# Performance work log

Hardware: AMD Instinct MI355X
Metric: run time of the kernel (lower is better)

Reference implementation:

```python
import jax, jax.numpy as jnp
import numpy as np

HEAD_NUMS = 8
LN_EPS = 1e-5


def _layernorm(x, g, b):
    m = jnp.mean(x, axis=-1, keepdims=True)
    v = jnp.var(x, axis=-1, keepdims=True)
    return (x - m) * jax.lax.rsqrt(v + LN_EPS) * g + b


def setup_inputs() -> dict:
    key = jax.random.key(0)
    ks = jax.random.split(key, 6)
    B, S, D = 4, 2048, 512
    x = jax.random.normal(ks[0], (B, S, D), dtype=jnp.float32)
    W1 = jax.random.normal(ks[1], (4 * D, D), dtype=jnp.float32) * 0.02
    b1 = jnp.zeros((4 * D,), dtype=jnp.float32)
    ln_g = jnp.ones((D,), dtype=jnp.float32)
    ln_b = jnp.zeros((D,), dtype=jnp.float32)
    W2 = jax.random.normal(ks[2], (D, D), dtype=jnp.float32) * 0.02
    b2 = jnp.zeros((D,), dtype=jnp.float32)
    return {"x": x, "W1": W1, "b1": b1, "ln_g": ln_g, "ln_b": ln_b, "W2": W2, "b2": b2}


def reference(x, W1, b1, ln_g, ln_b, W2, b2):
    B, S, D = x.shape
    H = HEAD_NUMS
    hd = D // H
    # fused qkv+gate projection with SiLU (HSTU style)
    h = jax.nn.silu(x @ W1.T + b1)                   # [B,S,4D]
    h = h.reshape(B, S, 4, H, hd)                    # split into gate,q,k,v
    gate = jnp.transpose(h[:, :, 0], (0, 2, 1, 3))   # [B,H,S,hd]
    q = jnp.transpose(h[:, :, 1], (0, 2, 1, 3))
    k = jnp.transpose(h[:, :, 2], (0, 2, 1, 3))
    v = jnp.transpose(h[:, :, 3], (0, 2, 1, 3))
    scale = 1.0 / np.sqrt(hd).astype(np.float32)
    scores = jnp.einsum('bhsd,bhtd->bhst', q, k) * scale   # [B,H,S,S]
    causal = jnp.tril(jnp.ones((S, S), dtype=bool))        # allowed: t <= s
    # silu replaces softmax; masked (future) positions contribute 0
    # (mathematical limit of silu(-inf) is 0)
    a = jnp.where(causal, jax.nn.silu(scores), 0.0)
    o = jnp.einsum('bhst,bhtd->bhsd', a, v)                # [B,H,S,hd]
    o = jnp.transpose(o, (0, 2, 1, 3)).reshape(B, S, D)
    normed = _layernorm(o, ln_g, ln_b)
    gate_f = jnp.transpose(gate, (0, 2, 1, 3)).reshape(B, S, D)
    return (normed * gate_f) @ W2.T + b2
```

## Files before the change

kernel.cpp:

```cpp
#include <hip/hip_runtime.h>
#include <hip/hip_bf16.h>
#include <cstdint>


typedef __attribute__((ext_vector_type(8))) short short8;
typedef __attribute__((ext_vector_type(4))) float f32x4;

__device__ __forceinline__ unsigned short f2bf(float f) {
  union { float f; unsigned u; } v; v.f = f;
  unsigned r = v.u + 0x7FFFu + ((v.u >> 16) & 1u);
  return (unsigned short)(r >> 16);
}
__device__ __forceinline__ float bf2f(unsigned short h) {
  union { unsigned u; float f; } v; v.u = ((unsigned)h) << 16; return v.f;
}
__device__ __forceinline__ float fast_rcp(float x) {
#if __has_builtin(__builtin_amdgcn_rcpf)
  return __builtin_amdgcn_rcpf(x);
#else
  return 1.0f / x;
#endif
}
__device__ __forceinline__ float fast_exp2(float x) {
#if __has_builtin(__builtin_amdgcn_exp2f)
  return __builtin_amdgcn_exp2f(x);
#else
  return exp2f(x);
#endif
}
__device__ __forceinline__ float silu_f(float x) {
  return x * fast_rcp(1.0f + fast_exp2(-1.442695041f * x));
}
__device__ __forceinline__ unsigned pk2(float lo, float hi) {
  union { __hip_bfloat162 b; unsigned u; } cv;
  cv.b = __float22bfloat162_rn(make_float2(lo, hi));
  return cv.u;
}
__device__ __forceinline__ void gl_lds16(const void* g, void* l) {
  __builtin_amdgcn_global_load_lds(
      (const __attribute__((address_space(1))) void*)g,
      (__attribute__((address_space(3))) void*)l, 16, 0, 0);
}

__global__ void convert_kernel(const float* __restrict__ x, const float* __restrict__ w1,
                               const float* __restrict__ w2,
                               unsigned short* __restrict__ xb, unsigned short* __restrict__ w1b,
                               unsigned short* __restrict__ w2b) {
  int i = blockIdx.x * 256 + threadIdx.x;
  const float* s; unsigned short* d;
  if (i < 1048576) { s = x; d = xb; }
  else if (i < 1048576 + 262144) { i -= 1048576; s = w1; d = w1b; }
  else { i -= (1048576 + 262144); if (i >= 65536) return; s = w2; d = w2b; }
  float4 f = ((const float4*)s)[i];
  uint2 o; o.x = pk2(f.x, f.y); o.y = pk2(f.z, f.w);
  ((uint2*)d)[i] = o;
}

__global__ __launch_bounds__(256, 2) void gemm1_kernel(
    const unsigned short* __restrict__ xb,
    const unsigned short* __restrict__ w1b,
    const float* __restrict__ b1,
    unsigned short* __restrict__ h,
    unsigned short* __restrict__ vt)
{
  __shared__ __align__(16) unsigned short smem[16896];
  unsigned short* As = smem;
  unsigned short* Bs = smem + 8192;
  const int tid = threadIdx.x;
  const int w = tid >> 6, l = tid & 63;
  const int bm = blockIdx.x & 63, bn = blockIdx.x >> 6;
  const int wm = w & 1, wn = w >> 1;
  const int quad = l >> 4, lc = l & 15, lc7 = lc & 7;
  const int r8 = l >> 3, c8 = (l & 7) ^ r8;

  f32x4 acc[4][4] = {};
  const unsigned short* ga = xb + (size_t)(bm * 128 + w * 32 + r8) * 512 + c8 * 8;
  const unsigned short* gb = w1b + (size_t)(bn * 128 + w * 32 + r8) * 512 + c8 * 8;

  for (int kt = 0; kt < 512; kt += 64) {
#pragma unroll
    for (int i = 0; i < 4; ++i) {
      gl_lds16(ga + i * 8 * 512 + kt, As + (w * 4 + i) * 512);
      gl_lds16(gb + i * 8 * 512 + kt, Bs + (w * 4 + i) * 512);
    }
    __syncthreads();
#pragma unroll
    for (int kk = 0; kk < 2; ++kk) {
      short8 af[4], bf[4];
#pragma unroll
      for (int mt = 0; mt < 4; ++mt)
        af[mt] = *(const short8*)(As + (wm * 64 + mt * 16 + lc) * 64 +
                                  (((kk * 4 + quad) ^ lc7) * 8));
#pragma unroll
      for (int nt = 0; nt < 4; ++nt)
        bf[nt] = *(const short8*)(Bs + (wn * 64 + nt * 16 + lc) * 64 +
                                  (((kk * 4 + quad) ^ lc7) * 8));
#pragma unroll
      for (int mt = 0; mt < 4; ++mt)
#pragma unroll
        for (int nt = 0; nt < 4; ++nt)
          acc[mt][nt] = __builtin_amdgcn_mfma_f32_16x16x32_bf16(af[mt], bf[nt], acc[mt][nt], 0, 0, 0);
    }
    __syncthreads();
  }

  unsigned short* T = smem;
  const int sec = bn >> 2;
  if (sec == 3) {
#pragma unroll
    for (int nt = 0; nt < 4; ++nt) {
      const int nl = wn * 64 + nt * 16 + lc;
      const float bias = b1[bn * 128 + nl];
#pragma unroll
      for (int mt = 0; mt < 4; ++mt) {
        const int sl = wm * 64 + mt * 16 + quad * 4;
        uint2 pk;
        pk.x = pk2(silu_f(acc[mt][nt][0] + bias), silu_f(acc[mt][nt][1] + bias));
        pk.y = pk2(silu_f(acc[mt][nt][2] + bias), silu_f(acc[mt][nt][3] + bias));
        *(uint2*)(T + nl * 132 + sl) = pk;
      }
    }
  } else {
    const float osc = (sec == 1) ? 0.125f : 1.0f;
#pragma unroll
    for (int nt = 0; nt < 4; ++nt) {
      const int nl = wn * 64 + nt * 16 + lc;
      const float bias = b1[bn * 128 + nl];
#pragma unroll
      for (int mt = 0; mt < 4; ++mt) {
        const int sl = wm * 64 + mt * 16 + quad * 4;
#pragma unroll
        for (int r = 0; r < 4; ++r)
          T[(sl + r) * 132 + nl] = f2bf(silu_f(acc[mt][nt][r] + bias) * osc);
      }
    }
  }
  __syncthreads();
  const int rrow = tid >> 4, rcol = (tid & 15) * 8;
  if (sec == 3) {
    const int bq = bm >> 4, sbase = (bm & 15) * 128;
#pragma unroll
    for (int p = 0; p < 8; ++p) {
      const int row = p * 16 + rrow;
      const int n = bn * 128 + row, hh = (n >> 6) & 7, d = n & 63;
      *(short8*)(vt + (size_t)((bq * 8 + hh) * 64 + d) * 2048 + sbase + rcol) =
          *(const short8*)(T + row * 132 + rcol);
    }
  } else {
#pragma unroll
    for (int p = 0; p < 8; ++p) {
      const int row = p * 16 + rrow;
      *(short8*)(h + (size_t)(bm * 128 + row) * 2048 + bn * 128 + rcol) =
          *(const short8*)(T + row * 132 + rcol);
    }
  }
}

__global__ __launch_bounds__(256, 3) void attn_kernel(
    const unsigned short* __restrict__ h,
    const unsigned short* __restrict__ vt,
    float* __restrict__ o)
{
  __shared__ __align__(16) unsigned short Ks[128 * 64];
  __shared__ __align__(16) unsigned short Vs[64 * 128];
  __shared__ __align__(16) unsigned short Ps[64 * 136];
  const int tid = threadIdx.x;
  const int w = tid >> 6, l = tid & 63;
  const int bh = blockIdx.x & 31;
  const int qi = 31 - (blockIdx.x >> 5);
  const int b = bh >> 3, hh = bh & 7;
  const int quad = l >> 4, lc = l & 15, lc7 = lc & 7;
  const int r8 = l >> 3, c8 = (l & 7) ^ r8;
  const int wm = w & 1, wn = w >> 1;
  const int q0 = qi * 64;
  const int nk = (qi >> 1) + 1;

  {
    const unsigned short* qg =
        h + (size_t)(b * 2048 + q0 + w * 16 + r8) * 2048 + 512 + hh * 64 + c8 * 8;
#pragma unroll
    for (int i = 0; i < 2; ++i)
      gl_lds16(qg + (size_t)i * 8 * 2048, Ks + (w * 2 + i) * 512);
  }
  __syncthreads();
  short8 qf[2][2];
#pragma unroll
  for (int nt = 0; nt < 2; ++nt)
#pragma unroll
    for (int kk = 0; kk < 2; ++kk)
      qf[nt][kk] = *(const short8*)(Ks + (wn * 32 + nt * 16 + lc) * 64 +
                                    (((kk * 4 + quad) ^ lc7) * 8));

  f32x4 oacc[4] = {};

  const unsigned short* kg =
      h + (size_t)(b * 2048 + w * 32 + r8) * 2048 + 1024 + hh * 64 + c8 * 8;
  const int vrow = l >> 4, vcol = l & 15;
  const unsigned short* vgE =
      vt + (size_t)(bh * 64 + w * 16 + vrow) * 2048 + ((vcol ^ vrow) * 8);
  const unsigned short* vgO =
      vt + (size_t)(bh * 64 + w * 16 + vrow) * 2048 + ((vcol ^ vrow ^ 4) * 8);

  for (int ti = 0; ti < nk; ++ti) {
    __syncthreads();
    const int toff = ti * 128;
#pragma unroll
    for (int i = 0; i < 4; ++i) {
      gl_lds16(kg + (size_t)(toff + i * 8) * 2048, Ks + (w * 4 + i) * 512);
      const unsigned short* vsrc = ((i & 1) ? vgO : vgE) + (size_t)(i * 4) * 2048 + toff;
      gl_lds16(vsrc, Vs + (w * 4 + i) * 512);
    }
    __syncthreads();

    f32x4 sc[4][2] = {};
#pragma unroll
    for (int kk = 0; kk < 2; ++kk) {
      short8 kf[4];
#pragma unroll
      for (int mt = 0; mt < 4; ++mt)
        kf[mt] = *(const short8*)(Ks + (wm * 64 + mt * 16 + lc) * 64 +
                                  (((kk * 4 + quad) ^ lc7) * 8));
#pragma unroll
      for (int mt = 0; mt < 4; ++mt)
#pragma unroll
        for (int nt = 0; nt < 2; ++nt)
          sc[mt][nt] = __builtin_amdgcn_mfma_f32_16x16x32_bf16(kf[mt], qf[nt][kk], sc[mt][nt], 0, 0, 0);
    }

    if (ti < nk - 1) {
#pragma unroll
      for (int mt = 0; mt < 4; ++mt) {
        const int tloc = wm * 64 + mt * 16 + quad * 4;
#pragma unroll
        for (int nt = 0; nt < 2; ++nt) {
          const int qloc = wn * 32 + nt * 16 + lc;
          uint2 pk;
          pk.x = pk2(silu_f(sc[mt][nt][0]), silu_f(sc[mt][nt][1]));
          pk.y = pk2(silu_f(sc[mt][nt][2]), silu_f(sc[mt][nt][3]));
          *(uint2*)(Ps + qloc * 136 + tloc) = pk;
        }
      }
    } else {
#pragma unroll
      for (int mt = 0; mt < 4; ++mt) {
        const int tloc = wm * 64 + mt * 16 + quad * 4;
        const int tg = toff + tloc;
#pragma unroll
        for (int nt = 0; nt < 2; ++nt) {
          const int qloc = wn * 32 + nt * 16 + lc;
          const int qg = q0 + qloc;
          float v0 = (tg + 0 <= qg) ? silu_f(sc[mt][nt][0]) : 0.0f;
          float v1 = (tg + 1 <= qg) ? silu_f(sc[mt][nt][1]) : 0.0f;
          float v2 = (tg + 2 <= qg) ? silu_f(sc[mt][nt][2]) : 0.0f;
          float v3 = (tg + 3 <= qg) ? silu_f(sc[mt][nt][3]) : 0.0f;
          uint2 pk; pk.x = pk2(v0, v1); pk.y = pk2(v2, v3);
          *(uint2*)(Ps + qloc * 136 + tloc) = pk;
        }
      }
    }
    __syncthreads();

#pragma unroll
    for (int ks = 0; ks < 4; ++ks) {
      short8 pf = *(const short8*)(Ps + (w * 16 + lc) * 136 + ks * 32 + quad * 8);
#pragma unroll
      for (int nt = 0; nt < 4; ++nt) {
        short8 vf = *(const short8*)(Vs + (nt * 16 + lc) * 128 +
                                     (((ks * 4 + quad) ^ lc7) * 8));
        oacc[nt] = __builtin_amdgcn_mfma_f32_16x16x32_bf16(pf, vf, oacc[nt], 0, 0, 0);
      }
    }
  }

  float* og = o + (size_t)(b * 2048 + q0 + w * 16) * 512 + hh * 64;
#pragma unroll
  for (int nt = 0; nt < 4; ++nt)
#pragma unroll
    for (int r = 0; r < 4; ++r)
      og[(quad * 4 + r) * 512 + nt * 16 + lc] = oacc[nt][r];
}

__global__ __launch_bounds__(256) void ln_gate_kernel(
    const float* __restrict__ o, const unsigned short* __restrict__ h,
    const float* __restrict__ lng, const float* __restrict__ lnb,
    unsigned short* __restrict__ y) {
  const int row = blockIdx.x * 4 + (threadIdx.x >> 6);
  const int l = threadIdx.x & 63;
  const float4* orow = (const float4*)(o + (size_t)row * 512);
  float4 a = orow[l * 2], c = orow[l * 2 + 1];
  float s0 = a.x + a.y + a.z + a.w + c.x + c.y + c.z + c.w;
#pragma unroll
  for (int off = 32; off > 0; off >>= 1) s0 += __shfl_xor(s0, off);
  const float mean = s0 * (1.0f / 512.0f);
  float dx[8] = {a.x - mean, a.y - mean, a.z - mean, a.w - mean,
                 c.x - mean, c.y - mean, c.z - mean, c.w - mean};
  float sq = 0.f;
#pragma unroll
  for (int j = 0; j < 8; ++j) sq += dx[j] * dx[j];
#pragma unroll
  for (int off = 32; off > 0; off >>= 1) sq += __shfl_xor(sq, off);
  const float inv = rsqrtf(sq * (1.0f / 512.0f) + 1e-5f);
  const float4* g4 = (const float4*)lng;
  const float4* b4 = (const float4*)lnb;
  float4 g0 = g4[l * 2], g1 = g4[l * 2 + 1], bb0 = b4[l * 2], bb1 = b4[l * 2 + 1];
  const unsigned short* grow = h + (size_t)row * 2048;
  ushort4 gr0 = *(const ushort4*)(grow + l * 8);
  ushort4 gr1 = *(const ushort4*)(grow + l * 8 + 4);
  float gg[8] = {g0.x, g0.y, g0.z, g0.w, g1.x, g1.y, g1.z, g1.w};
  float bbv[8] = {bb0.x, bb0.y, bb0.z, bb0.w, bb1.x, bb1.y, bb1.z, bb1.w};
  float gv[8] = {bf2f(gr0.x), bf2f(gr0.y), bf2f(gr0.z), bf2f(gr0.w),
                 bf2f(gr1.x), bf2f(gr1.y), bf2f(gr1.z), bf2f(gr1.w)};
  float r[8];
#pragma unroll
  for (int j = 0; j < 8; ++j) r[j] = (dx[j] * inv * gg[j] + bbv[j]) * gv[j];
  uint2 p0, p1;
  p0.x = pk2(r[0], r[1]); p0.y = pk2(r[2], r[3]);
  p1.x = pk2(r[4], r[5]); p1.y = pk2(r[6], r[7]);
  uint2* yrow = (uint2*)(y + (size_t)row * 512);
  yrow[l * 2] = p0;
  yrow[l * 2 + 1] = p1;
}

__global__ __launch_bounds__(256, 2) void gemm2_kernel(
    const unsigned short* __restrict__ yb,
    const unsigned short* __restrict__ w2b,
    const float* __restrict__ b2, float* __restrict__ out) {
  __shared__ __align__(16) unsigned short As[128 * 64];
  __shared__ __align__(16) unsigned short Bs[128 * 64];
  const int tid = threadIdx.x;
  const int w = tid >> 6, l = tid & 63;
  const int bm = blockIdx.x & 63, bn = blockIdx.x >> 6;
  const int wm = w & 1, wn = w >> 1;
  const int quad = l >> 4, lc = l & 15, lc7 = lc & 7;
  const int r8 = l >> 3, c8 = (l & 7) ^ r8;

  f32x4 acc[4][4] = {};
  const unsigned short* ga = yb + (size_t)(bm * 128 + w * 32 + r8) * 512 + c8 * 8;
  const unsigned short* gb = w2b + (size_t)(bn * 128 + w * 32 + r8) * 512 + c8 * 8;

  for (int kt = 0; kt < 512; kt += 64) {
#pragma unroll
    for (int i = 0; i < 4; ++i) {
      gl_lds16(ga + i * 8 * 512 + kt, As + (w * 4 + i) * 512);
      gl_lds16(gb + i * 8 * 512 + kt, Bs + (w * 4 + i) * 512);
    }
    __syncthreads();
#pragma unroll
    for (int kk = 0; kk < 2; ++kk) {
      short8 af[4], bf[4];
#pragma unroll
      for (int mt = 0; mt < 4; ++mt)
        af[mt] = *(const short8*)(As + (wm * 64 + mt * 16 + lc) * 64 +
                                  (((kk * 4 + quad) ^ lc7) * 8));
#pragma unroll
      for (int nt = 0; nt < 4; ++nt)
        bf[nt] = *(const short8*)(Bs + (wn * 64 + nt * 16 + lc) * 64 +
                                  (((kk * 4 + quad) ^ lc7) * 8));
#pragma unroll
      for (int mt = 0; mt < 4; ++mt)
#pragma unroll
        for (int nt = 0; nt < 4; ++nt)
          acc[mt][nt] = __builtin_amdgcn_mfma_f32_16x16x32_bf16(af[mt], bf[nt], acc[mt][nt], 0, 0, 0);
    }
    __syncthreads();
  }

#pragma unroll
  for (int nt = 0; nt < 4; ++nt) {
    const int n = bn * 128 + wn * 64 + nt * 16 + lc;
    const float bias = b2[n];
#pragma unroll
    for (int mt = 0; mt < 4; ++mt) {
      const int m0 = bm * 128 + wm * 64 + mt * 16 + quad * 4;
#pragma unroll
      for (int r = 0; r < 4; ++r)
        out[(size_t)(m0 + r) * 512 + n] = acc[mt][nt][r] + bias;
    }
  }
}

extern "C" void kernel_launch(void* const* d_in, const int* in_sizes, int n_in,
                              void* d_out, int out_size, void* d_ws, size_t ws_size,
                              hipStream_t stream) {
  const float* x = (const float*)d_in[0];
  const float* W1 = (const float*)d_in[1];
  const float* b1 = (const float*)d_in[2];
  const float* lng = (const float*)d_in[3];
  const float* lnb = (const float*)d_in[4];
  const float* W2 = (const float*)d_in[5];
  const float* b2 = (const float*)d_in[6];
  float* out = (float*)d_out;
  char* ws = (char*)d_ws;

  unsigned short* xb  = (unsigned short*)(ws);
  unsigned short* w1b = (unsigned short*)(ws + 8388608);
  unsigned short* w2b = (unsigned short*)(ws + 10485760);
  unsigned short* h   = (unsigned short*)(ws + 11010048);
  unsigned short* vt  = (unsigned short*)(ws + 44564480);
  float* o            = (float*)(ws + 52953088);
  unsigned short* yb  = (unsigned short*)(ws + 69730304);

  convert_kernel<<<5376, 256, 0, stream>>>(x, W1, W2, xb, w1b, w2b);
  gemm1_kernel<<<1024, 256, 0, stream>>>(xb, w1b, b1, h, vt);
  attn_kernel<<<1024, 256, 0, stream>>>(h, vt, o);
  ln_gate_kernel<<<2048, 256, 0, stream>>>(o, h, lng, lnb, yb);
  gemm2_kernel<<<256, 256, 0, stream>>>(yb, w2b, b2, out);
}
```

Measured before the change: 158.9 us.

## Register-prefetch next K/V tile in attention; shrink gemm2 tiles for more blocks

In the attention kernel, the direct global-to-LDS loads of K and V are replaced by a register prefetch. The next tile's K and V are loaded into registers while the current tile is computed, then written to LDS at the start of the next iteration. This is meant to hide global load latency behind the MFMA and SiLU work, at the cost of extra VGPRs and an extra register-to-LDS store. Separately, gemm2 uses 64x128 tiles with 512 blocks instead of 128x128 with 256, to better fill the CUs for this small GEMM at the cost of less reuse per block.

```diff
diff --git a/kernel.cpp b/kernel.cpp
--- a/kernel.cpp
+++ b/kernel.cpp
@@ -193,24 +193,39 @@
 
   f32x4 oacc[4] = {};
 
-  const unsigned short* kg =
+  const unsigned short* kgl =
       h + (size_t)(b * 2048 + w * 32 + r8) * 2048 + 1024 + hh * 64 + c8 * 8;
   const int vrow = l >> 4, vcol = l & 15;
-  const unsigned short* vgE =
-      vt + (size_t)(bh * 64 + w * 16 + vrow) * 2048 + ((vcol ^ vrow) * 8);
-  const unsigned short* vgO =
-      vt + (size_t)(bh * 64 + w * 16 + vrow) * 2048 + ((vcol ^ vrow ^ 4) * 8);
+  const unsigned short* vgl[4];
+#pragma unroll
+  for (int i = 0; i < 4; ++i) {
+    const int d = w * 16 + i * 4 + vrow;
+    vgl[i] = vt + (size_t)(bh * 64 + d) * 2048 + ((vcol ^ (d & 7)) * 8);
+  }
+
+  short8 kreg[4], vreg[4];
+#pragma unroll
+  for (int i = 0; i < 4; ++i) {
+    kreg[i] = *(const short8*)(kgl + (size_t)(i * 8) * 2048);
+    vreg[i] = *(const short8*)(vgl[i]);
+  }
 
   for (int ti = 0; ti < nk; ++ti) {
     __syncthreads();
-    const int toff = ti * 128;
 #pragma unroll
     for (int i = 0; i < 4; ++i) {
-      gl_lds16(kg + (size_t)(toff + i * 8) * 2048, Ks + (w * 4 + i) * 512);
-      const unsigned short* vsrc = ((i & 1) ? vgO : vgE) + (size_t)(i * 4) * 2048 + toff;
-      gl_lds16(vsrc, Vs + (w * 4 + i) * 512);
-    }
-    __syncthreads();
+      *(short8*)(Ks + (w * 4 + i) * 512 + l * 8) = kreg[i];
+      *(short8*)(Vs + (w * 4 + i) * 512 + l * 8) = vreg[i];
+    }
+    __syncthreads();
+    if (ti + 1 < nk) {
+      const int toff = (ti + 1) * 128;
+#pragma unroll
+      for (int i = 0; i < 4; ++i) {
+        kreg[i] = *(const short8*)(kgl + (size_t)(toff + i * 8) * 2048);
+        vreg[i] = *(const short8*)(vgl[i] + toff);
+      }
+    }
 
     f32x4 sc[4][2] = {};
 #pragma unroll
@@ -241,6 +256,7 @@
         }
       }
     } else {
+      const int toff = ti * 128;
 #pragma unroll
       for (int mt = 0; mt < 4; ++mt) {
         const int tloc = wm * 64 + mt * 16 + quad * 4;
@@ -325,53 +341,52 @@
     const unsigned short* __restrict__ yb,
     const unsigned short* __restrict__ w2b,
     const float* __restrict__ b2, float* __restrict__ out) {
-  __shared__ __align__(16) unsigned short As[128 * 64];
+  __shared__ __align__(16) unsigned short As[64 * 64];
   __shared__ __align__(16) unsigned short Bs[128 * 64];
   const int tid = threadIdx.x;
   const int w = tid >> 6, l = tid & 63;
-  const int bm = blockIdx.x & 63, bn = blockIdx.x >> 6;
-  const int wm = w & 1, wn = w >> 1;
+  const int bm = blockIdx.x & 127, bn = blockIdx.x >> 7;
   const int quad = l >> 4, lc = l & 15, lc7 = lc & 7;
   const int r8 = l >> 3, c8 = (l & 7) ^ r8;
 
-  f32x4 acc[4][4] = {};
-  const unsigned short* ga = yb + (size_t)(bm * 128 + w * 32 + r8) * 512 + c8 * 8;
+  f32x4 acc[4][2] = {};
+  const unsigned short* ga = yb + (size_t)(bm * 64 + w * 16 + r8) * 512 + c8 * 8;
   const unsigned short* gb = w2b + (size_t)(bn * 128 + w * 32 + r8) * 512 + c8 * 8;
 
   for (int kt = 0; kt < 512; kt += 64) {
 #pragma unroll
-    for (int i = 0; i < 4; ++i) {
-      gl_lds16(ga + i * 8 * 512 + kt, As + (w * 4 + i) * 512);
-      gl_lds16(gb + i * 8 * 512 + kt, Bs + (w * 4 + i) * 512);
-    }
+    for (int j = 0; j < 2; ++j)
+      gl_lds16(ga + j * 8 * 512 + kt, As + (w * 2 + j) * 512);
+#pragma unroll
+    for (int j = 0; j < 4; ++j)
+      gl_lds16(gb + j * 8 * 512 + kt, Bs + (w * 4 + j) * 512);
     __syncthreads();
 #pragma unroll
     for (int kk = 0; kk < 2; ++kk) {
-      short8 af[4], bf[4];
-#pragma unroll
-      for (int mt = 0; mt < 4; ++mt)
-        af[mt] = *(const short8*)(As + (wm * 64 + mt * 16 + lc) * 64 +
+      short8 af[4], bf[2];
+#pragma unroll
+      for (int mt = 0; mt < 4; ++mt)
+        af[mt] = *(const short8*)(As + (mt * 16 + lc) * 64 + (((kk * 4 + quad) ^ lc7) * 8));
+#pragma unroll
+      for (int nt = 0; nt < 2; ++nt)
+        bf[nt] = *(const short8*)(Bs + (w * 32 + nt * 16 + lc) * 64 +
                                   (((kk * 4 + quad) ^ lc7) * 8));
 #pragma unroll
-      for (int nt = 0; nt < 4; ++nt)
-        bf[nt] = *(const short8*)(Bs + (wn * 64 + nt * 16 + lc) * 64 +
-                                  (((kk * 4 + quad) ^ lc7) * 8));
-#pragma unroll
-      for (int mt = 0; mt < 4; ++mt)
-#pragma unroll
-        for (int nt = 0; nt < 4; ++nt)
+      for (int mt = 0; mt < 4; ++mt)
+#pragma unroll
+        for (int nt = 0; nt < 2; ++nt)
           acc[mt][nt] = __builtin_amdgcn_mfma_f32_16x16x32_bf16(af[mt], bf[nt], acc[mt][nt], 0, 0, 0);
     }
     __syncthreads();
   }
 
 #pragma unroll
-  for (int nt = 0; nt < 4; ++nt) {
-    const int n = bn * 128 + wn * 64 + nt * 16 + lc;
+  for (int nt = 0; nt < 2; ++nt) {
+    const int n = bn * 128 + w * 32 + nt * 16 + lc;
     const float bias = b2[n];
 #pragma unroll
     for (int mt = 0; mt < 4; ++mt) {
-      const int m0 = bm * 128 + wm * 64 + mt * 16 + quad * 4;
+      const int m0 = bm * 64 + mt * 16 + quad * 4;
 #pragma unroll
       for (int r = 0; r < 4; ++r)
         out[(size_t)(m0 + r) * 512 + n] = acc[mt][nt][r] + bias;
@@ -404,5 +419,5 @@
   gemm1_kernel<<<1024, 256, 0, stream>>>(xb, w1b, b1, h, vt);
   attn_kernel<<<1024, 256, 0, stream>>>(h, vt, o);
   ln_gate_kernel<<<2048, 256, 0, stream>>>(o, h, lng, lnb, yb);
-  gemm2_kernel<<<256, 256, 0, stream>>>(yb, w2b, b2, out);
-}
+  gemm2_kernel<<<512, 256, 0, stream>>>(yb, w2b, b2, out);
+}
```

Measured after the change: 159.5 us. About the same (+0.3%).
